# Optimization experiments

Measured on AMD Instinct MI355X. Metric: run time of the kernel, lower is better.

## Reference

```python
import jax, jax.numpy as jnp
import numpy as np

NEG_INF = jnp.float32(-jnp.inf)

def setup_inputs() -> dict:
    key = jax.random.key(0)
    kq, kk, kv = jax.random.split(key, 3)
    shape = (2, 16, 2048, 64)  # [batch, heads, seq, head_dim]
    q = jax.random.normal(kq, shape, dtype=jnp.float32)
    k = jax.random.normal(kk, shape, dtype=jnp.float32)
    v = jax.random.normal(kv, shape, dtype=jnp.float32)
    return {"q": q, "k": k, "v": v}

def reference(q, k, v):
    seq_len = q.shape[-2]
    scale = q.shape[-1] ** 0.5
    # scores: [b, h, s, s]
    scores = jnp.einsum('bhqd,bhkd->bhqk', q, k)
    causal_mask = jnp.triu(jnp.ones((seq_len, seq_len), dtype=bool), k=1)
    scores = jnp.where(causal_mask, NEG_INF, scores)
    weights = jax.nn.softmax(scores / scale, axis=-1)
    out = jnp.einsum('bhqk,bhkd->bhqd', weights, v)
    return out
```

## Files before the change

kernel.cpp:

```cpp
#include <hip/hip_runtime.h>
#include <hip/hip_bf16.h>
#include <cstdint>

#define SEQ   2048
#define HD    64
#define NBH   32
#define QBLK  64
#define KVBLK 64
#define NQT   (SEQ / QBLK)
#define LDK   72
#define QSC   0.18033688011112042f
#define THR   11.0f

typedef __attribute__((ext_vector_type(8))) short short8;
typedef __attribute__((ext_vector_type(4))) float floatx4;

#if __has_builtin(__builtin_amdgcn_exp2f)
#define EXP2(x) __builtin_amdgcn_exp2f(x)
#else
#define EXP2(x) __expf((x) * 0.69314718055994531f)
#endif

static __device__ __forceinline__ short f2bf(float f) {
    union { float f; unsigned u; } x; x.f = f;
    return (short)((x.u + 0x7fffu + ((x.u >> 16) & 1u)) >> 16);
}
static __device__ __forceinline__ unsigned pkbf(float a, float b) {
    __hip_bfloat162 h = __float22bfloat162_rn(make_float2(a, b));
    union { __hip_bfloat162 h; unsigned u; } c; c.h = h; return c.u;
}


__global__ __launch_bounds__(256)
void conv_k_kernel(const float* __restrict__ K, short* __restrict__ Kb) {
    size_t i = ((size_t)blockIdx.x * 256 + threadIdx.x) * 8;
    float4 a = *(const float4*)(K + i);
    float4 b = *(const float4*)(K + i + 4);
    union { unsigned u[4]; short8 s; } cv;
    cv.u[0] = pkbf(a.x, a.y); cv.u[1] = pkbf(a.z, a.w);
    cv.u[2] = pkbf(b.x, b.y); cv.u[3] = pkbf(b.z, b.w);
    *(short8*)(Kb + i) = cv.s;
}

__global__ __launch_bounds__(256)
void trans_v_kernel(const float* __restrict__ V, short* __restrict__ Vt) {
    __shared__ __align__(16) short Vs[64][72];
    const int tid = threadIdx.x;
    const int bh = blockIdx.x >> 5;
    const int t  = blockIdx.x & 31;
    const float* src = V + ((size_t)bh * SEQ + (size_t)t * 64) * HD;
    #pragma unroll
    for (int i = 0; i < 4; ++i) {
        int idx = i * 256 + tid;
        int r = idx >> 4; int c = (idx & 15) * 4;
        float4 f = *(const float4*)(src + r * HD + c);
        Vs[c + 0][r] = f2bf(f.x); Vs[c + 1][r] = f2bf(f.y);
        Vs[c + 2][r] = f2bf(f.z); Vs[c + 3][r] = f2bf(f.w);
    }
    __syncthreads();
    short* dst = Vt + (size_t)bh * HD * SEQ + t * 64;
    #pragma unroll
    for (int i = 0; i < 2; ++i) {
        int idx = i * 256 + tid;
        int d = idx >> 3; int j = idx & 7;
        short8 v = *(const short8*)&Vs[d][j * 8];
        *(short8*)(dst + (size_t)d * SEQ + j * 8) = v;
    }
}


__global__ __launch_bounds__(256, 4)
void fa_fwd_v9(const float* __restrict__ Q, const short* __restrict__ Kg,
               const short* __restrict__ Vtg, float* __restrict__ O)
{
    const int tid  = threadIdx.x;
    const int lane = tid & 63;
    const int wv   = tid >> 6;
    const int l15  = lane & 15;
    const int lg   = lane >> 4;
    const int lg4  = lg * 4;
    const int dofs = lg * 8;

    const int bh = blockIdx.x & (NBH - 1);
    const int qi = (NQT - 1) - (blockIdx.x >> 5);
    const int qbase = qi * QBLK;

    const float* Qp = Q   + (size_t)bh * SEQ * HD;
    const short* Kp = Kg  + (size_t)bh * SEQ * HD;
    const short* Vp = Vtg + (size_t)bh * HD * SEQ;
    float*       Op = O   + (size_t)bh * SEQ * HD;

    __shared__ __align__(16) short K_lds[2][KVBLK][LDK];
    __shared__ __align__(16) short Vt_lds[2][HD][LDK];

    const int r0 = tid >> 3,         j0 = tid & 7;
    const int r1 = (tid + 256) >> 3, j1 = tid & 7;
    const int kg0 = r0 * HD + j0 * 8, kg1 = r1 * HD + j1 * 8;
    const int vg0 = r0 * SEQ + j0 * 8, vg1 = r1 * SEQ + j1 * 8;

    const int rowb = ((l15 & ~3) << 1) + (l15 & 3);
    const int kb   = 8 * lg;

    short8 qf0, qf1;
    {
        const float* src = Qp + (size_t)(qbase + wv * 16 + l15) * HD + dofs;
        union { unsigned u[4]; short8 s; } cv;
        float4 f0 = *(const float4*)(src);
        float4 f1 = *(const float4*)(src + 4);
        cv.u[0] = pkbf(f0.x * QSC, f0.y * QSC); cv.u[1] = pkbf(f0.z * QSC, f0.w * QSC);
        cv.u[2] = pkbf(f1.x * QSC, f1.y * QSC); cv.u[3] = pkbf(f1.z * QSC, f1.w * QSC);
        qf0 = cv.s;
        f0 = *(const float4*)(src + 32);
        f1 = *(const float4*)(src + 36);
        cv.u[0] = pkbf(f0.x * QSC, f0.y * QSC); cv.u[1] = pkbf(f0.z * QSC, f0.w * QSC);
        cv.u[2] = pkbf(f1.x * QSC, f1.y * QSC); cv.u[3] = pkbf(f1.z * QSC, f1.w * QSC);
        qf1 = cv.s;
    }

    short8 krA = *(const short8*)(Kp + kg0);
    short8 krB = *(const short8*)(Kp + kg1);
    short8 vrA = *(const short8*)(Vp + vg0);
    short8 vrB = *(const short8*)(Vp + vg1);

    floatx4 o_acc[4];
    #pragma unroll
    for (int dt = 0; dt < 4; ++dt)
        #pragma unroll
        for (int e = 0; e < 4; ++e) o_acc[dt][e] = 0.0f;
    float m_s = -1e30f, l_s = 0.0f;

    for (int t = 0; t <= qi; ++t) {
        const int buf = t & 1;
        *(short8*)&K_lds[buf][r0][j0 * 8]  = krA;
        *(short8*)&K_lds[buf][r1][j1 * 8]  = krB;
        *(short8*)&Vt_lds[buf][r0][j0 * 8] = vrA;
        *(short8*)&Vt_lds[buf][r1][j1 * 8] = vrB;
        __syncthreads();

        if (t < qi) {
            const short* ks = Kp + (size_t)(t + 1) * KVBLK * HD;
            const short* vs = Vp + (t + 1) * KVBLK;
            krA = *(const short8*)(ks + kg0);
            krB = *(const short8*)(ks + kg1);
            vrA = *(const short8*)(vs + vg0);
            vrB = *(const short8*)(vs + vg1);
        }

        const int roff[4] = {0, 4, 32, 36};
        floatx4 s_acc[4];
        __builtin_amdgcn_s_setprio(1);
        #pragma unroll
        for (int n = 0; n < 4; ++n) {
            const short* krow = &K_lds[buf][rowb + roff[n]][0];
            const short8 k0 = *(const short8*)(krow + dofs);
            const short8 k1 = *(const short8*)(krow + dofs + 32);
            floatx4 acc = {0.0f, 0.0f, 0.0f, 0.0f};
            acc = __builtin_amdgcn_mfma_f32_16x16x32_bf16(k0, qf0, acc, 0, 0, 0);
            acc = __builtin_amdgcn_mfma_f32_16x16x32_bf16(k1, qf1, acc, 0, 0, 0);
            s_acc[n] = acc;
        }
        __builtin_amdgcn_s_setprio(0);

        if (t == qi) {
            const int qlocal = wv * 16 + l15;
            #pragma unroll
            for (int n = 0; n < 4; ++n)
                #pragma unroll
                for (int r = 0; r < 4; ++r)
                    if (kb + roff[n] + r > qlocal) s_acc[n][r] = -1e30f;
        }

        float t0 = fmaxf(fmaxf(s_acc[0][0], s_acc[0][1]), fmaxf(s_acc[0][2], s_acc[0][3]));
        float t1 = fmaxf(fmaxf(s_acc[1][0], s_acc[1][1]), fmaxf(s_acc[1][2], s_acc[1][3]));
        float t2 = fmaxf(fmaxf(s_acc[2][0], s_acc[2][1]), fmaxf(s_acc[2][2], s_acc[2][3]));
        float t3 = fmaxf(fmaxf(s_acc[3][0], s_acc[3][1]), fmaxf(s_acc[3][2], s_acc[3][3]));
        float rmax = fmaxf(fmaxf(t0, t1), fmaxf(t2, t3));
        rmax = fmaxf(rmax, __shfl_xor(rmax, 16));
        rmax = fmaxf(rmax, __shfl_xor(rmax, 32));

        const bool trig = rmax > m_s + THR;
        float alpha = 1.0f;
        if (trig) {
            alpha = EXP2(m_s - rmax);
            m_s = rmax;
            l_s *= alpha;
        }
        if (__any(trig)) {
            float a0 = __shfl(alpha, lg4 + 0);
            float a1 = __shfl(alpha, lg4 + 1);
            float a2 = __shfl(alpha, lg4 + 2);
            float a3 = __shfl(alpha, lg4 + 3);
            #pragma unroll
            for (int dt = 0; dt < 4; ++dt) {
                o_acc[dt][0] *= a0; o_acc[dt][1] *= a1;
                o_acc[dt][2] *= a2; o_acc[dt][3] *= a3;
            }
        }

        short8 p0, p1;
        {
            float p00 = EXP2(s_acc[0][0] - m_s), p01 = EXP2(s_acc[0][1] - m_s);
            float p02 = EXP2(s_acc[0][2] - m_s), p03 = EXP2(s_acc[0][3] - m_s);
            float p10 = EXP2(s_acc[1][0] - m_s), p11 = EXP2(s_acc[1][1] - m_s);
            float p12 = EXP2(s_acc[1][2] - m_s), p13 = EXP2(s_acc[1][3] - m_s);
            float p20 = EXP2(s_acc[2][0] - m_s), p21 = EXP2(s_acc[2][1] - m_s);
            float p22 = EXP2(s_acc[2][2] - m_s), p23 = EXP2(s_acc[2][3] - m_s);
            float p30 = EXP2(s_acc[3][0] - m_s), p31 = EXP2(s_acc[3][1] - m_s);
            float p32 = EXP2(s_acc[3][2] - m_s), p33 = EXP2(s_acc[3][3] - m_s);
            l_s += ((p00 + p01) + (p02 + p03)) + ((p10 + p11) + (p12 + p13))
                 + ((p20 + p21) + (p22 + p23)) + ((p30 + p31) + (p32 + p33));
            union { unsigned u[4]; short8 s; } c0, c1;
            c0.u[0] = pkbf(p00, p01); c0.u[1] = pkbf(p02, p03);
            c0.u[2] = pkbf(p10, p11); c0.u[3] = pkbf(p12, p13);
            c1.u[0] = pkbf(p20, p21); c1.u[1] = pkbf(p22, p23);
            c1.u[2] = pkbf(p30, p31); c1.u[3] = pkbf(p32, p33);
            p0 = c0.s; p1 = c1.s;
        }

        __builtin_amdgcn_s_setprio(1);
        #pragma unroll
        for (int dt = 0; dt < 4; ++dt) {
            const short8 v0 = *(const short8*)&Vt_lds[buf][dt * 16 + l15][dofs];
            const short8 v1 = *(const short8*)&Vt_lds[buf][dt * 16 + l15][dofs + 32];
            o_acc[dt] = __builtin_amdgcn_mfma_f32_16x16x32_bf16(p0, v0, o_acc[dt], 0, 0, 0);
            o_acc[dt] = __builtin_amdgcn_mfma_f32_16x16x32_bf16(p1, v1, o_acc[dt], 0, 0, 0);
        }
        __builtin_amdgcn_s_setprio(0);
    }

    l_s += __shfl_xor(l_s, 16);
    l_s += __shfl_xor(l_s, 32);
    const float linv = 1.0f / l_s;
    #pragma unroll
    for (int e = 0; e < 4; ++e) {
        const float li = __shfl(linv, lg4 + e);
        const int row = qbase + wv * 16 + lg4 + e;
        #pragma unroll
        for (int dt = 0; dt < 4; ++dt)
            Op[(size_t)row * HD + dt * 16 + l15] = o_acc[dt][e] * li;
    }
}


__global__ __launch_bounds__(256, 2)
void fa_fwd_v1(const float* __restrict__ Q, const float* __restrict__ K,
               const float* __restrict__ V, float* __restrict__ O)
{
    const int tid  = threadIdx.x;
    const int lane = tid & 63;
    const int wv   = tid >> 6;
    const int l15  = lane & 15;
    const int lg   = lane >> 4;
    const int dofs = lg * 8;
    const int bh = blockIdx.x & (NBH - 1);
    const int qi = 31 - (blockIdx.x >> 5);
    const size_t base = (size_t)bh * SEQ * HD;
    const float* Qp = Q + base; const float* Kp = K + base;
    const float* Vp = V + base; float* Op = O + base;
    const int qbase = qi * 64;
    __shared__ __align__(16) short K_lds[64][72];
    __shared__ __align__(16) short Vt_lds[HD][72];
    __shared__ __align__(16) short P_lds[4][16][72];
    short8 qfrag[2];
    {
        const float* src = Qp + (size_t)(qbase + wv * 16 + l15) * HD + dofs;
        #pragma unroll
        for (int c = 0; c < 2; ++c) {
            float4 f0 = *(const float4*)(src + 32 * c);
            float4 f1 = *(const float4*)(src + 32 * c + 4);
            short8 tt;
            tt[0] = f2bf(f0.x * 0.125f); tt[1] = f2bf(f0.y * 0.125f);
            tt[2] = f2bf(f0.z * 0.125f); tt[3] = f2bf(f0.w * 0.125f);
            tt[4] = f2bf(f1.x * 0.125f); tt[5] = f2bf(f1.y * 0.125f);
            tt[6] = f2bf(f1.z * 0.125f); tt[7] = f2bf(f1.w * 0.125f);
            qfrag[c] = tt;
        }
    }
    floatx4 o_acc[4];
    #pragma unroll
    for (int dt = 0; dt < 4; ++dt)
        #pragma unroll
        for (int e = 0; e < 4; ++e) o_acc[dt][e] = 0.0f;
    float m_r[4], l_r[4];
    #pragma unroll
    for (int r = 0; r < 4; ++r) { m_r[r] = -1e30f; l_r[r] = 0.0f; }
    for (int t = 0; t <= qi; ++t) {
        __syncthreads();
        {
            const float4* ks = (const float4*)(Kp + (size_t)t * 64 * HD);
            const float4* vs = (const float4*)(Vp + (size_t)t * 64 * HD);
            #pragma unroll
            for (int j = 0; j < 4; ++j) {
                int idx = j * 256 + tid;
                int row = idx >> 4;
                int col = (idx & 15) << 2;
                float4 kf = ks[idx];
                K_lds[row][col + 0] = f2bf(kf.x); K_lds[row][col + 1] = f2bf(kf.y);
                K_lds[row][col + 2] = f2bf(kf.z); K_lds[row][col + 3] = f2bf(kf.w);
                float4 vf = vs[idx];
                Vt_lds[col + 0][row] = f2bf(vf.x); Vt_lds[col + 1][row] = f2bf(vf.y);
                Vt_lds[col + 2][row] = f2bf(vf.z); Vt_lds[col + 3][row] = f2bf(vf.w);
            }
        }
        __syncthreads();
        floatx4 s_acc[4];
        #pragma unroll
        for (int n = 0; n < 4; ++n) {
            const short8 k0 = *(const short8*)&K_lds[n * 16 + l15][dofs];
            const short8 k1 = *(const short8*)&K_lds[n * 16 + l15][dofs + 32];
            floatx4 acc = {0.0f, 0.0f, 0.0f, 0.0f};
            acc = __builtin_amdgcn_mfma_f32_16x16x32_bf16(qfrag[0], k0, acc, 0, 0, 0);
            acc = __builtin_amdgcn_mfma_f32_16x16x32_bf16(qfrag[1], k1, acc, 0, 0, 0);
            s_acc[n] = acc;
        }
        if (t == qi) {
            #pragma unroll
            for (int n = 0; n < 4; ++n)
                #pragma unroll
                for (int r = 0; r < 4; ++r) {
                    int qr = wv * 16 + lg * 4 + r;
                    int kc = n * 16 + l15;
                    if (kc > qr) s_acc[n][r] = -1e30f;
                }
        }
        #pragma unroll
        for (int r = 0; r < 4; ++r) {
            float rmax = fmaxf(fmaxf(s_acc[0][r], s_acc[1][r]),
                               fmaxf(s_acc[2][r], s_acc[3][r]));
            rmax = fmaxf(rmax, __shfl_xor(rmax, 1));
            rmax = fmaxf(rmax, __shfl_xor(rmax, 2));
            rmax = fmaxf(rmax, __shfl_xor(rmax, 4));
            rmax = fmaxf(rmax, __shfl_xor(rmax, 8));
            float mnew  = fmaxf(m_r[r], rmax);
            float alpha = __expf(m_r[r] - mnew);
            m_r[r] = mnew;
            l_r[r] *= alpha;
            #pragma unroll
            for (int dt = 0; dt < 4; ++dt) o_acc[dt][r] *= alpha;
            #pragma unroll
            for (int n = 0; n < 4; ++n) {
                float p = __expf(s_acc[n][r] - mnew);
                l_r[r] += p;
                P_lds[wv][lg * 4 + r][n * 16 + l15] = f2bf(p);
            }
        }
        asm volatile("s_waitcnt lgkmcnt(0)" ::: "memory");
        const short8 p0 = *(const short8*)&P_lds[wv][l15][dofs];
        const short8 p1 = *(const short8*)&P_lds[wv][l15][dofs + 32];
        #pragma unroll
        for (int dt = 0; dt < 4; ++dt) {
            const short8 v0 = *(const short8*)&Vt_lds[dt * 16 + l15][dofs];
            const short8 v1 = *(const short8*)&Vt_lds[dt * 16 + l15][dofs + 32];
            o_acc[dt] = __builtin_amdgcn_mfma_f32_16x16x32_bf16(p0, v0, o_acc[dt], 0, 0, 0);
            o_acc[dt] = __builtin_amdgcn_mfma_f32_16x16x32_bf16(p1, v1, o_acc[dt], 0, 0, 0);
        }
    }
    #pragma unroll
    for (int r = 0; r < 4; ++r) {
        float l = l_r[r];
        l += __shfl_xor(l, 1);
        l += __shfl_xor(l, 2);
        l += __shfl_xor(l, 4);
        l += __shfl_xor(l, 8);
        l_r[r] = 1.0f / l;
    }
    #pragma unroll
    for (int dt = 0; dt < 4; ++dt)
        #pragma unroll
        for (int r = 0; r < 4; ++r) {
            int row = qbase + wv * 16 + lg * 4 + r;
            Op[(size_t)row * HD + dt * 16 + l15] = o_acc[dt][r] * l_r[r];
        }
}

extern "C" void kernel_launch(void* const* d_in, const int* in_sizes, int n_in,
                              void* d_out, int out_size, void* d_ws, size_t ws_size,
                              hipStream_t stream) {
    const float* q = (const float*)d_in[0];
    const float* k = (const float*)d_in[1];
    const float* v = (const float*)d_in[2];
    float* o = (float*)d_out;
    (void)in_sizes; (void)n_in; (void)out_size;

    const size_t elems = (size_t)NBH * SEQ * HD;
    const size_t need  = 2 * elems * sizeof(short);
    if (ws_size >= need) {
        short* kb = (short*)d_ws;
        short* vt = kb + elems;
        conv_k_kernel<<<dim3(elems / (256 * 8)), dim3(256), 0, stream>>>(k, kb);
        trans_v_kernel<<<dim3(NBH * 32), dim3(256), 0, stream>>>(v, vt);
        fa_fwd_v9<<<dim3(NBH * NQT), dim3(256), 0, stream>>>(q, kb, vt, o);
    } else {
        fa_fwd_v1<<<dim3(NBH * 32), dim3(256), 0, stream>>>(q, k, v, o);
    }
}
```

Measured before the change: 53.77 us.

## Load V fragments directly from global and speculatively compute softmax exponentials

Removes the V tile from shared memory: each lane now loads its MFMA B-operand V fragments straight from the pre-transposed global Vt at the start of each iteration, without the register prefetch. It also computes the exponentials against the old running max before the row max is known, and recomputes them only on lanes whose max rose past the threshold. The aim is to cut LDS traffic and footprint and to shorten the dependency chain between the max reduction and the exponentials. In exchange, V loads are exposed to global/L2 latency with no double buffering, and a rescale event costs twice the exponentials.

```diff
diff --git a/kernel.cpp b/kernel.cpp
--- a/kernel.cpp
+++ b/kernel.cpp
@@ -70,8 +70,8 @@
 
 
 __global__ __launch_bounds__(256, 4)
-void fa_fwd_v9(const float* __restrict__ Q, const short* __restrict__ Kg,
-               const short* __restrict__ Vtg, float* __restrict__ O)
+void fa_fwd_v10(const float* __restrict__ Q, const short* __restrict__ Kg,
+                const short* __restrict__ Vtg, float* __restrict__ O)
 {
     const int tid  = threadIdx.x;
     const int lane = tid & 63;
@@ -91,12 +91,10 @@
     float*       Op = O   + (size_t)bh * SEQ * HD;
 
     __shared__ __align__(16) short K_lds[2][KVBLK][LDK];
-    __shared__ __align__(16) short Vt_lds[2][HD][LDK];
 
     const int r0 = tid >> 3,         j0 = tid & 7;
     const int r1 = (tid + 256) >> 3, j1 = tid & 7;
     const int kg0 = r0 * HD + j0 * 8, kg1 = r1 * HD + j1 * 8;
-    const int vg0 = r0 * SEQ + j0 * 8, vg1 = r1 * SEQ + j1 * 8;
 
     const int rowb = ((l15 & ~3) << 1) + (l15 & 3);
     const int kb   = 8 * lg;
@@ -119,8 +117,6 @@
 
     short8 krA = *(const short8*)(Kp + kg0);
     short8 krB = *(const short8*)(Kp + kg1);
-    short8 vrA = *(const short8*)(Vp + vg0);
-    short8 vrB = *(const short8*)(Vp + vg1);
 
     floatx4 o_acc[4];
     #pragma unroll
@@ -131,19 +127,22 @@
 
     for (int t = 0; t <= qi; ++t) {
         const int buf = t & 1;
-        *(short8*)&K_lds[buf][r0][j0 * 8]  = krA;
-        *(short8*)&K_lds[buf][r1][j1 * 8]  = krB;
-        *(short8*)&Vt_lds[buf][r0][j0 * 8] = vrA;
-        *(short8*)&Vt_lds[buf][r1][j1 * 8] = vrB;
+        *(short8*)&K_lds[buf][r0][j0 * 8] = krA;
+        *(short8*)&K_lds[buf][r1][j1 * 8] = krB;
         __syncthreads();
+
+        short8 vA[4], vB[4];
+        #pragma unroll
+        for (int dt = 0; dt < 4; ++dt) {
+            const short* vr = Vp + (size_t)(dt * 16 + l15) * SEQ + t * KVBLK + dofs;
+            vA[dt] = *(const short8*)(vr);
+            vB[dt] = *(const short8*)(vr + 32);
+        }
 
         if (t < qi) {
             const short* ks = Kp + (size_t)(t + 1) * KVBLK * HD;
-            const short* vs = Vp + (t + 1) * KVBLK;
             krA = *(const short8*)(ks + kg0);
             krB = *(const short8*)(ks + kg1);
-            vrA = *(const short8*)(vs + vg0);
-            vrB = *(const short8*)(vs + vg1);
         }
 
         const int roff[4] = {0, 4, 32, 36};
@@ -170,6 +169,17 @@
                     if (kb + roff[n] + r > qlocal) s_acc[n][r] = -1e30f;
         }
 
+        float p00 = EXP2(s_acc[0][0] - m_s), p01 = EXP2(s_acc[0][1] - m_s);
+        float p02 = EXP2(s_acc[0][2] - m_s), p03 = EXP2(s_acc[0][3] - m_s);
+        float p10 = EXP2(s_acc[1][0] - m_s), p11 = EXP2(s_acc[1][1] - m_s);
+        float p12 = EXP2(s_acc[1][2] - m_s), p13 = EXP2(s_acc[1][3] - m_s);
+        float p20 = EXP2(s_acc[2][0] - m_s), p21 = EXP2(s_acc[2][1] - m_s);
+        float p22 = EXP2(s_acc[2][2] - m_s), p23 = EXP2(s_acc[2][3] - m_s);
+        float p30 = EXP2(s_acc[3][0] - m_s), p31 = EXP2(s_acc[3][1] - m_s);
+        float p32 = EXP2(s_acc[3][2] - m_s), p33 = EXP2(s_acc[3][3] - m_s);
+        float lsum = ((p00 + p01) + (p02 + p03)) + ((p10 + p11) + (p12 + p13))
+                   + ((p20 + p21) + (p22 + p23)) + ((p30 + p31) + (p32 + p33));
+
         float t0 = fmaxf(fmaxf(s_acc[0][0], s_acc[0][1]), fmaxf(s_acc[0][2], s_acc[0][3]));
         float t1 = fmaxf(fmaxf(s_acc[1][0], s_acc[1][1]), fmaxf(s_acc[1][2], s_acc[1][3]));
         float t2 = fmaxf(fmaxf(s_acc[2][0], s_acc[2][1]), fmaxf(s_acc[2][2], s_acc[2][3]));
@@ -179,13 +189,23 @@
         rmax = fmaxf(rmax, __shfl_xor(rmax, 32));
 
         const bool trig = rmax > m_s + THR;
-        float alpha = 1.0f;
-        if (trig) {
-            alpha = EXP2(m_s - rmax);
-            m_s = rmax;
-            l_s *= alpha;
-        }
         if (__any(trig)) {
+            float alpha = 1.0f;
+            if (trig) {
+                alpha = EXP2(m_s - rmax);
+                m_s = rmax;
+                p00 = EXP2(s_acc[0][0] - m_s); p01 = EXP2(s_acc[0][1] - m_s);
+                p02 = EXP2(s_acc[0][2] - m_s); p03 = EXP2(s_acc[0][3] - m_s);
+                p10 = EXP2(s_acc[1][0] - m_s); p11 = EXP2(s_acc[1][1] - m_s);
+                p12 = EXP2(s_acc[1][2] - m_s); p13 = EXP2(s_acc[1][3] - m_s);
+                p20 = EXP2(s_acc[2][0] - m_s); p21 = EXP2(s_acc[2][1] - m_s);
+                p22 = EXP2(s_acc[2][2] - m_s); p23 = EXP2(s_acc[2][3] - m_s);
+                p30 = EXP2(s_acc[3][0] - m_s); p31 = EXP2(s_acc[3][1] - m_s);
+                p32 = EXP2(s_acc[3][2] - m_s); p33 = EXP2(s_acc[3][3] - m_s);
+                lsum = ((p00 + p01) + (p02 + p03)) + ((p10 + p11) + (p12 + p13))
+                     + ((p20 + p21) + (p22 + p23)) + ((p30 + p31) + (p32 + p33));
+            }
+            l_s = l_s * alpha + lsum;
             float a0 = __shfl(alpha, lg4 + 0);
             float a1 = __shfl(alpha, lg4 + 1);
             float a2 = __shfl(alpha, lg4 + 2);
@@ -195,20 +215,12 @@
                 o_acc[dt][0] *= a0; o_acc[dt][1] *= a1;
                 o_acc[dt][2] *= a2; o_acc[dt][3] *= a3;
             }
+        } else {
+            l_s += lsum;
         }
 
         short8 p0, p1;
         {
-            float p00 = EXP2(s_acc[0][0] - m_s), p01 = EXP2(s_acc[0][1] - m_s);
-            float p02 = EXP2(s_acc[0][2] - m_s), p03 = EXP2(s_acc[0][3] - m_s);
-            float p10 = EXP2(s_acc[1][0] - m_s), p11 = EXP2(s_acc[1][1] - m_s);
-            float p12 = EXP2(s_acc[1][2] - m_s), p13 = EXP2(s_acc[1][3] - m_s);
-            float p20 = EXP2(s_acc[2][0] - m_s), p21 = EXP2(s_acc[2][1] - m_s);
-            float p22 = EXP2(s_acc[2][2] - m_s), p23 = EXP2(s_acc[2][3] - m_s);
-            float p30 = EXP2(s_acc[3][0] - m_s), p31 = EXP2(s_acc[3][1] - m_s);
-            float p32 = EXP2(s_acc[3][2] - m_s), p33 = EXP2(s_acc[3][3] - m_s);
-            l_s += ((p00 + p01) + (p02 + p03)) + ((p10 + p11) + (p12 + p13))
-                 + ((p20 + p21) + (p22 + p23)) + ((p30 + p31) + (p32 + p33));
             union { unsigned u[4]; short8 s; } c0, c1;
             c0.u[0] = pkbf(p00, p01); c0.u[1] = pkbf(p02, p03);
             c0.u[2] = pkbf(p10, p11); c0.u[3] = pkbf(p12, p13);
@@ -220,10 +232,8 @@
         __builtin_amdgcn_s_setprio(1);
         #pragma unroll
         for (int dt = 0; dt < 4; ++dt) {
-            const short8 v0 = *(const short8*)&Vt_lds[buf][dt * 16 + l15][dofs];
-            const short8 v1 = *(const short8*)&Vt_lds[buf][dt * 16 + l15][dofs + 32];
-            o_acc[dt] = __builtin_amdgcn_mfma_f32_16x16x32_bf16(p0, v0, o_acc[dt], 0, 0, 0);
-            o_acc[dt] = __builtin_amdgcn_mfma_f32_16x16x32_bf16(p1, v1, o_acc[dt], 0, 0, 0);
+            o_acc[dt] = __builtin_amdgcn_mfma_f32_16x16x32_bf16(p0, vA[dt], o_acc[dt], 0, 0, 0);
+            o_acc[dt] = __builtin_amdgcn_mfma_f32_16x16x32_bf16(p1, vB[dt], o_acc[dt], 0, 0, 0);
         }
         __builtin_amdgcn_s_setprio(0);
     }
@@ -389,7 +399,7 @@
         short* vt = kb + elems;
         conv_k_kernel<<<dim3(elems / (256 * 8)), dim3(256), 0, stream>>>(k, kb);
         trans_v_kernel<<<dim3(NBH * 32), dim3(256), 0, stream>>>(v, vt);
-        fa_fwd_v9<<<dim3(NBH * NQT), dim3(256), 0, stream>>>(q, kb, vt, o);
+        fa_fwd_v10<<<dim3(NBH * NQT), dim3(256), 0, stream>>>(q, kb, vt, o);
     } else {
         fa_fwd_v1<<<dim3(NBH * 32), dim3(256), 0, stream>>>(q, k, v, o);
     }
```

After: 137.0 us. 155% more time.

## Process two 16-row query groups per wave with 128-thread blocks

Applied to the files above, without the earlier changes.

Halves the block to two waves, each handling 32 query rows as two 16-row groups that share the K fragments loaded from LDS and the V fragments in the PV MFMAs. This doubles register-level reuse of K/V fragments, cutting LDS reads per MFMA. In exchange each block has fewer waves to hide latency, per-thread global staging loads double, and register pressure rises with two sets of accumulators and softmax state. Launch bounds move to 128 threads with a min of 2 blocks.

```diff
diff --git a/kernel.cpp b/kernel.cpp
--- a/kernel.cpp
+++ b/kernel.cpp
@@ -69,9 +69,9 @@
 }
 
 
-__global__ __launch_bounds__(256, 4)
-void fa_fwd_v9(const float* __restrict__ Q, const short* __restrict__ Kg,
-               const short* __restrict__ Vtg, float* __restrict__ O)
+__global__ __launch_bounds__(128, 2)
+void fa_fwd_v12(const float* __restrict__ Q, const short* __restrict__ Kg,
+                const short* __restrict__ Vtg, float* __restrict__ O)
 {
     const int tid  = threadIdx.x;
     const int lane = tid & 63;
@@ -93,128 +93,141 @@
     __shared__ __align__(16) short K_lds[2][KVBLK][LDK];
     __shared__ __align__(16) short Vt_lds[2][HD][LDK];
 
-    const int r0 = tid >> 3,         j0 = tid & 7;
-    const int r1 = (tid + 256) >> 3, j1 = tid & 7;
-    const int kg0 = r0 * HD + j0 * 8, kg1 = r1 * HD + j1 * 8;
-    const int vg0 = r0 * SEQ + j0 * 8, vg1 = r1 * SEQ + j1 * 8;
+    const int sr = tid >> 3;
+    const int sj = (tid & 7) * 8;
 
     const int rowb = ((l15 & ~3) << 1) + (l15 & 3);
     const int kb   = 8 * lg;
 
-    short8 qf0, qf1;
-    {
-        const float* src = Qp + (size_t)(qbase + wv * 16 + l15) * HD + dofs;
+    short8 qf[2][2];
+    #pragma unroll
+    for (int g = 0; g < 2; ++g) {
+        const float* src = Qp + (size_t)(qbase + wv * 32 + g * 16 + l15) * HD + dofs;
         union { unsigned u[4]; short8 s; } cv;
         float4 f0 = *(const float4*)(src);
         float4 f1 = *(const float4*)(src + 4);
         cv.u[0] = pkbf(f0.x * QSC, f0.y * QSC); cv.u[1] = pkbf(f0.z * QSC, f0.w * QSC);
         cv.u[2] = pkbf(f1.x * QSC, f1.y * QSC); cv.u[3] = pkbf(f1.z * QSC, f1.w * QSC);
-        qf0 = cv.s;
+        qf[g][0] = cv.s;
         f0 = *(const float4*)(src + 32);
         f1 = *(const float4*)(src + 36);
         cv.u[0] = pkbf(f0.x * QSC, f0.y * QSC); cv.u[1] = pkbf(f0.z * QSC, f0.w * QSC);
         cv.u[2] = pkbf(f1.x * QSC, f1.y * QSC); cv.u[3] = pkbf(f1.z * QSC, f1.w * QSC);
-        qf1 = cv.s;
-    }
-
-    short8 krA = *(const short8*)(Kp + kg0);
-    short8 krB = *(const short8*)(Kp + kg1);
-    short8 vrA = *(const short8*)(Vp + vg0);
-    short8 vrB = *(const short8*)(Vp + vg1);
-
-    floatx4 o_acc[4];
-    #pragma unroll
-    for (int dt = 0; dt < 4; ++dt)
-        #pragma unroll
-        for (int e = 0; e < 4; ++e) o_acc[dt][e] = 0.0f;
-    float m_s = -1e30f, l_s = 0.0f;
+        qf[g][1] = cv.s;
+    }
+
+    short8 kr[4], vr[4];
+    #pragma unroll
+    for (int i = 0; i < 4; ++i) {
+        kr[i] = *(const short8*)(Kp + (size_t)(sr + i * 16) * HD + sj);
+        vr[i] = *(const short8*)(Vp + (size_t)(sr + i * 16) * SEQ + sj);
+    }
+
+    floatx4 o_acc[2][4];
+    #pragma unroll
+    for (int g = 0; g < 2; ++g)
+        #pragma unroll
+        for (int dt = 0; dt < 4; ++dt)
+            #pragma unroll
+            for (int e = 0; e < 4; ++e) o_acc[g][dt][e] = 0.0f;
+    float m_s[2] = {-1e30f, -1e30f};
+    float l_s[2] = {0.0f, 0.0f};
 
     for (int t = 0; t <= qi; ++t) {
         const int buf = t & 1;
-        *(short8*)&K_lds[buf][r0][j0 * 8]  = krA;
-        *(short8*)&K_lds[buf][r1][j1 * 8]  = krB;
-        *(short8*)&Vt_lds[buf][r0][j0 * 8] = vrA;
-        *(short8*)&Vt_lds[buf][r1][j1 * 8] = vrB;
+        #pragma unroll
+        for (int i = 0; i < 4; ++i) {
+            *(short8*)&K_lds[buf][sr + i * 16][sj]  = kr[i];
+            *(short8*)&Vt_lds[buf][sr + i * 16][sj] = vr[i];
+        }
         __syncthreads();
 
         if (t < qi) {
             const short* ks = Kp + (size_t)(t + 1) * KVBLK * HD;
             const short* vs = Vp + (t + 1) * KVBLK;
-            krA = *(const short8*)(ks + kg0);
-            krB = *(const short8*)(ks + kg1);
-            vrA = *(const short8*)(vs + vg0);
-            vrB = *(const short8*)(vs + vg1);
+            #pragma unroll
+            for (int i = 0; i < 4; ++i) {
+                kr[i] = *(const short8*)(ks + (size_t)(sr + i * 16) * HD + sj);
+                vr[i] = *(const short8*)(vs + (size_t)(sr + i * 16) * SEQ + sj);
+            }
         }
 
         const int roff[4] = {0, 4, 32, 36};
-        floatx4 s_acc[4];
-        __builtin_amdgcn_s_setprio(1);
+        short8 kf0[4], kf1[4];
         #pragma unroll
         for (int n = 0; n < 4; ++n) {
             const short* krow = &K_lds[buf][rowb + roff[n]][0];
-            const short8 k0 = *(const short8*)(krow + dofs);
-            const short8 k1 = *(const short8*)(krow + dofs + 32);
-            floatx4 acc = {0.0f, 0.0f, 0.0f, 0.0f};
-            acc = __builtin_amdgcn_mfma_f32_16x16x32_bf16(k0, qf0, acc, 0, 0, 0);
-            acc = __builtin_amdgcn_mfma_f32_16x16x32_bf16(k1, qf1, acc, 0, 0, 0);
-            s_acc[n] = acc;
-        }
-        __builtin_amdgcn_s_setprio(0);
-
-        if (t == qi) {
-            const int qlocal = wv * 16 + l15;
-            #pragma unroll
-            for (int n = 0; n < 4; ++n)
+            kf0[n] = *(const short8*)(krow + dofs);
+            kf1[n] = *(const short8*)(krow + dofs + 32);
+        }
+
+        short8 pp[2][2];
+        #pragma unroll
+        for (int g = 0; g < 2; ++g) {
+            floatx4 s_acc[4];
+            __builtin_amdgcn_s_setprio(1);
+            #pragma unroll
+            for (int n = 0; n < 4; ++n) {
+                floatx4 acc = {0.0f, 0.0f, 0.0f, 0.0f};
+                acc = __builtin_amdgcn_mfma_f32_16x16x32_bf16(kf0[n], qf[g][0], acc, 0, 0, 0);
+                acc = __builtin_amdgcn_mfma_f32_16x16x32_bf16(kf1[n], qf[g][1], acc, 0, 0, 0);
+                s_acc[n] = acc;
+            }
+            __builtin_amdgcn_s_setprio(0);
+
+            if (t == qi) {
+                const int qlocal = wv * 32 + g * 16 + l15;
                 #pragma unroll
-                for (int r = 0; r < 4; ++r)
-                    if (kb + roff[n] + r > qlocal) s_acc[n][r] = -1e30f;
-        }
-
-        float t0 = fmaxf(fmaxf(s_acc[0][0], s_acc[0][1]), fmaxf(s_acc[0][2], s_acc[0][3]));
-        float t1 = fmaxf(fmaxf(s_acc[1][0], s_acc[1][1]), fmaxf(s_acc[1][2], s_acc[1][3]));
-        float t2 = fmaxf(fmaxf(s_acc[2][0], s_acc[2][1]), fmaxf(s_acc[2][2], s_acc[2][3]));
-        float t3 = fmaxf(fmaxf(s_acc[3][0], s_acc[3][1]), fmaxf(s_acc[3][2], s_acc[3][3]));
-        float rmax = fmaxf(fmaxf(t0, t1), fmaxf(t2, t3));
-        rmax = fmaxf(rmax, __shfl_xor(rmax, 16));
-        rmax = fmaxf(rmax, __shfl_xor(rmax, 32));
-
-        const bool trig = rmax > m_s + THR;
-        float alpha = 1.0f;
-        if (trig) {
-            alpha = EXP2(m_s - rmax);
-            m_s = rmax;
-            l_s *= alpha;
-        }
-        if (__any(trig)) {
-            float a0 = __shfl(alpha, lg4 + 0);
-            float a1 = __shfl(alpha, lg4 + 1);
-            float a2 = __shfl(alpha, lg4 + 2);
-            float a3 = __shfl(alpha, lg4 + 3);
-            #pragma unroll
-            for (int dt = 0; dt < 4; ++dt) {
-                o_acc[dt][0] *= a0; o_acc[dt][1] *= a1;
-                o_acc[dt][2] *= a2; o_acc[dt][3] *= a3;
-            }
-        }
-
-        short8 p0, p1;
-        {
-            float p00 = EXP2(s_acc[0][0] - m_s), p01 = EXP2(s_acc[0][1] - m_s);
-            float p02 = EXP2(s_acc[0][2] - m_s), p03 = EXP2(s_acc[0][3] - m_s);
-            float p10 = EXP2(s_acc[1][0] - m_s), p11 = EXP2(s_acc[1][1] - m_s);
-            float p12 = EXP2(s_acc[1][2] - m_s), p13 = EXP2(s_acc[1][3] - m_s);
-            float p20 = EXP2(s_acc[2][0] - m_s), p21 = EXP2(s_acc[2][1] - m_s);
-            float p22 = EXP2(s_acc[2][2] - m_s), p23 = EXP2(s_acc[2][3] - m_s);
-            float p30 = EXP2(s_acc[3][0] - m_s), p31 = EXP2(s_acc[3][1] - m_s);
-            float p32 = EXP2(s_acc[3][2] - m_s), p33 = EXP2(s_acc[3][3] - m_s);
-            l_s += ((p00 + p01) + (p02 + p03)) + ((p10 + p11) + (p12 + p13))
-                 + ((p20 + p21) + (p22 + p23)) + ((p30 + p31) + (p32 + p33));
+                for (int n = 0; n < 4; ++n)
+                    #pragma unroll
+                    for (int r = 0; r < 4; ++r)
+                        if (kb + roff[n] + r > qlocal) s_acc[n][r] = -1e30f;
+            }
+
+            float t0 = fmaxf(fmaxf(s_acc[0][0], s_acc[0][1]), fmaxf(s_acc[0][2], s_acc[0][3]));
+            float t1 = fmaxf(fmaxf(s_acc[1][0], s_acc[1][1]), fmaxf(s_acc[1][2], s_acc[1][3]));
+            float t2 = fmaxf(fmaxf(s_acc[2][0], s_acc[2][1]), fmaxf(s_acc[2][2], s_acc[2][3]));
+            float t3 = fmaxf(fmaxf(s_acc[3][0], s_acc[3][1]), fmaxf(s_acc[3][2], s_acc[3][3]));
+            float rmax = fmaxf(fmaxf(t0, t1), fmaxf(t2, t3));
+            rmax = fmaxf(rmax, __shfl_xor(rmax, 16));
+            rmax = fmaxf(rmax, __shfl_xor(rmax, 32));
+
+            const bool trig = rmax > m_s[g] + THR;
+            float alpha = 1.0f;
+            if (trig) {
+                alpha = EXP2(m_s[g] - rmax);
+                m_s[g] = rmax;
+                l_s[g] *= alpha;
+            }
+            if (__any(trig)) {
+                float a0 = __shfl(alpha, lg4 + 0);
+                float a1 = __shfl(alpha, lg4 + 1);
+                float a2 = __shfl(alpha, lg4 + 2);
+                float a3 = __shfl(alpha, lg4 + 3);
+                #pragma unroll
+                for (int dt = 0; dt < 4; ++dt) {
+                    o_acc[g][dt][0] *= a0; o_acc[g][dt][1] *= a1;
+                    o_acc[g][dt][2] *= a2; o_acc[g][dt][3] *= a3;
+                }
+            }
+
+            const float mm = m_s[g];
+            float p00 = EXP2(s_acc[0][0] - mm), p01 = EXP2(s_acc[0][1] - mm);
+            float p02 = EXP2(s_acc[0][2] - mm), p03 = EXP2(s_acc[0][3] - mm);
+            float p10 = EXP2(s_acc[1][0] - mm), p11 = EXP2(s_acc[1][1] - mm);
+            float p12 = EXP2(s_acc[1][2] - mm), p13 = EXP2(s_acc[1][3] - mm);
+            float p20 = EXP2(s_acc[2][0] - mm), p21 = EXP2(s_acc[2][1] - mm);
+            float p22 = EXP2(s_acc[2][2] - mm), p23 = EXP2(s_acc[2][3] - mm);
+            float p30 = EXP2(s_acc[3][0] - mm), p31 = EXP2(s_acc[3][1] - mm);
+            float p32 = EXP2(s_acc[3][2] - mm), p33 = EXP2(s_acc[3][3] - mm);
+            l_s[g] += ((p00 + p01) + (p02 + p03)) + ((p10 + p11) + (p12 + p13))
+                    + ((p20 + p21) + (p22 + p23)) + ((p30 + p31) + (p32 + p33));
             union { unsigned u[4]; short8 s; } c0, c1;
             c0.u[0] = pkbf(p00, p01); c0.u[1] = pkbf(p02, p03);
             c0.u[2] = pkbf(p10, p11); c0.u[3] = pkbf(p12, p13);
             c1.u[0] = pkbf(p20, p21); c1.u[1] = pkbf(p22, p23);
             c1.u[2] = pkbf(p30, p31); c1.u[3] = pkbf(p32, p33);
-            p0 = c0.s; p1 = c1.s;
+            pp[g][0] = c0.s; pp[g][1] = c1.s;
         }
 
         __builtin_amdgcn_s_setprio(1);
@@ -222,22 +235,28 @@
         for (int dt = 0; dt < 4; ++dt) {
             const short8 v0 = *(const short8*)&Vt_lds[buf][dt * 16 + l15][dofs];
             const short8 v1 = *(const short8*)&Vt_lds[buf][dt * 16 + l15][dofs + 32];
-            o_acc[dt] = __builtin_amdgcn_mfma_f32_16x16x32_bf16(p0, v0, o_acc[dt], 0, 0, 0);
-            o_acc[dt] = __builtin_amdgcn_mfma_f32_16x16x32_bf16(p1, v1, o_acc[dt], 0, 0, 0);
+            o_acc[0][dt] = __builtin_amdgcn_mfma_f32_16x16x32_bf16(pp[0][0], v0, o_acc[0][dt], 0, 0, 0);
+            o_acc[0][dt] = __builtin_amdgcn_mfma_f32_16x16x32_bf16(pp[0][1], v1, o_acc[0][dt], 0, 0, 0);
+            o_acc[1][dt] = __builtin_amdgcn_mfma_f32_16x16x32_bf16(pp[1][0], v0, o_acc[1][dt], 0, 0, 0);
+            o_acc[1][dt] = __builtin_amdgcn_mfma_f32_16x16x32_bf16(pp[1][1], v1, o_acc[1][dt], 0, 0, 0);
         }
         __builtin_amdgcn_s_setprio(0);
     }
 
-    l_s += __shfl_xor(l_s, 16);
-    l_s += __shfl_xor(l_s, 32);
-    const float linv = 1.0f / l_s;
-    #pragma unroll
-    for (int e = 0; e < 4; ++e) {
-        const float li = __shfl(linv, lg4 + e);
-        const int row = qbase + wv * 16 + lg4 + e;
-        #pragma unroll
-        for (int dt = 0; dt < 4; ++dt)
-            Op[(size_t)row * HD + dt * 16 + l15] = o_acc[dt][e] * li;
+    #pragma unroll
+    for (int g = 0; g < 2; ++g) {
+        float lt = l_s[g];
+        lt += __shfl_xor(lt, 16);
+        lt += __shfl_xor(lt, 32);
+        const float linv = 1.0f / lt;
+        #pragma unroll
+        for (int e = 0; e < 4; ++e) {
+            const float li = __shfl(linv, lg4 + e);
+            const int row = qbase + wv * 32 + g * 16 + lg4 + e;
+            #pragma unroll
+            for (int dt = 0; dt < 4; ++dt)
+                Op[(size_t)row * HD + dt * 16 + l15] = o_acc[g][dt][e] * li;
+        }
     }
 }
 
@@ -389,7 +408,7 @@
         short* vt = kb + elems;
         conv_k_kernel<<<dim3(elems / (256 * 8)), dim3(256), 0, stream>>>(k, kb);
         trans_v_kernel<<<dim3(NBH * 32), dim3(256), 0, stream>>>(v, vt);
-        fa_fwd_v9<<<dim3(NBH * NQT), dim3(256), 0, stream>>>(q, kb, vt, o);
+        fa_fwd_v12<<<dim3(NBH * NQT), dim3(128), 0, stream>>>(q, kb, vt, o);
     } else {
         fa_fwd_v1<<<dim3(NBH * 32), dim3(256), 0, stream>>>(q, k, v, o);
     }
```

Measured after the change: 63.98 us. 19.0% more time.
